# Kernel tuning notes

Measured on AMD Instinct MI355X. Metric: run time of the kernel, lower is better.

Reference implementation:

```python
import jax, jax.numpy as jnp
import numpy as np

B, C, H, W, K = 2, 64, 192, 192, 7
PAD = K // 2
EPS = 1e-6


def _win_idx(L):
    # NATTEN border handling: window is shifted (not zero-padded) to stay in-bounds.
    i = jnp.arange(L)
    start = jnp.clip(i - PAD, 0, L - K)            # [L] window start per query pos
    win = start[:, None] + jnp.arange(K)[None]     # [L,K] absolute key positions
    pb = (K - 1) - (i - start)                     # [L] rpb start index per query pos
    pbi = pb[:, None] + jnp.arange(K)[None]        # [L,K] rpb table indices
    return win, pbi


def setup_inputs() -> dict:
    key = jax.random.key(0)
    ks = jax.random.split(key, 10)
    g = jax.random.normal(ks[0], (B, C, H, W), jnp.float32)
    cd = jax.random.uniform(ks[1], (B, 1, H, W), dtype=jnp.float32)
    dense = jax.random.uniform(ks[2], (B, 1, H, W), dtype=jnp.float32)
    sel = jax.random.uniform(ks[3], (B, 1, H, W)) < 0.05
    sd = jnp.where(sel, dense, 0.0)
    mask = (jax.random.uniform(ks[4], (B, 1, H, W)) < 0.5).astype(jnp.float32)
    ln_w = 1.0 + 0.02 * jax.random.normal(ks[5], (C,), jnp.float32)
    ln_b = 0.02 * jax.random.normal(ks[6], (C,), jnp.float32)
    conv_w = 0.05 * jax.random.normal(ks[7], (2 * C, C + 1), jnp.float32)  # 1x1 conv
    conv_b = 0.02 * jax.random.normal(ks[8], (2 * C,), jnp.float32)
    rpb = 0.02 * jax.random.normal(ks[9], (1, 2 * K - 1, 2 * K - 1), jnp.float32)
    return {"g": g, "cd": cd, "sd": sd, "mask": mask,
            "ln_w": ln_w, "ln_b": ln_b, "conv_w": conv_w, "conv_b": conv_b, "rpb": rpb}


def reference(g, cd, sd, mask, ln_w, ln_b, conv_w, conv_b, rpb):
    # LayerNorm2d: normalize over channel dim per spatial location
    mu = g.mean(axis=1, keepdims=True)
    var = ((g - mu) ** 2).mean(axis=1, keepdims=True)
    gn = (g - mu) * jax.lax.rsqrt(var + EPS)
    gn = gn * ln_w[None, :, None, None] + ln_b[None, :, None, None]

    z = jnp.concatenate([gn, cd], axis=1)                      # [B,C+1,H,W]
    qk = jnp.einsum('bchw,oc->bohw', z, conv_w) + conv_b[None, :, None, None]
    q, k = qk[:, :C], qk[:, C:]
    k = k * mask

    qc = q.transpose(0, 2, 3, 1)                               # [B,H,W,C] single head
    kc = k.transpose(0, 2, 3, 1)
    rwin, rpbi = _win_idx(H)
    cwin, cpbi = _win_idx(W)

    # NATTEN qk + relative position bias over 7x7 neighborhoods
    k_win = kc[:, rwin][:, :, :, cwin]                         # [B,H,K,W,K,C]
    attn = jnp.einsum('bhwc,bhiwjc->bhwij', qc, k_win)         # [B,H,W,K,K]
    bias = rpb[0][rpbi][:, :, cpbi]                            # [H,K,W,K]
    attn = attn + bias.transpose(0, 2, 1, 3)[None]
    a = jax.nn.softmax(attn.reshape(B, H, W, K * K), axis=-1).reshape(B, H, W, K, K)

    # NATTEN av with v = cd (head_dim 1)
    v_win = cd[:, 0][:, rwin][:, :, :, cwin]                   # [B,H,K,W,K]
    cd_out = jnp.einsum('bhwij,bhiwj->bhw', a, v_win)[:, None]  # [B,1,H,W]
    m_win = mask[:, 0][:, rwin][:, :, :, cwin]
    mask_out = jnp.einsum('bhwij,bhiwj->bhw', a, m_win)[:, None]

    # NYU / SDR post-processing
    cd_out = cd_out * mask + cd * (1.0 - mask)
    valid = sd > 0
    cd_out = jnp.where(valid, sd, cd_out)
    mask_out = jnp.where(valid, mask, mask_out)
    return cd_out, mask_out
```

## Files before the change

kernel.cpp:

```cpp
#include <hip/hip_runtime.h>

constexpr int NB = 2;
constexpr int NC = 64;
constexpr int NH = 192;
constexpr int NW = 192;
constexpr int NK = 7;
constexpr int NHW = NH * NW;
constexpr int NPIX = NB * NHW;
constexpr float EPS = 1e-6f;

__global__ __launch_bounds__(256) void qk_gemm(
    const float* __restrict__ g, const float* __restrict__ cd,
    const float* __restrict__ mask,
    const float* __restrict__ ln_w, const float* __restrict__ ln_b,
    const float* __restrict__ conv_w, const float* __restrict__ conv_b,
    float* __restrict__ qbuf, float* __restrict__ kbuf)
{
    __shared__ float Z[65][128];
    __shared__ float WTc[33][128];

    int tid = threadIdx.x;
    int p0 = blockIdx.x * 128;
    int b  = p0 / NHW;
    int hw0 = p0 - b * NHW;

    int px = tid >> 1;
    int hf = tid & 1;
    const float* gp = g + (size_t)(b * NC + hf * 32) * NHW + (hw0 + px);
    float vals[32];
    float s = 0.f, sq = 0.f;
#pragma unroll
    for (int j = 0; j < 32; ++j) {
        float v = gp[(size_t)j * NHW];
        vals[j] = v; s += v; sq += v * v;
    }
    s  += __shfl_xor(s, 1);
    sq += __shfl_xor(sq, 1);
    float mu   = s * (1.f / 64.f);
    float rstd = rsqrtf(sq * (1.f / 64.f) - mu * mu + EPS);
#pragma unroll
    for (int j = 0; j < 32; ++j) {
        int c = hf * 32 + j;
        Z[c][px] = (vals[j] - mu) * rstd * ln_w[c] + ln_b[c];
    }
    if (hf) Z[64][px] = cd[p0 + px];

    int og = tid >> 4;
    int pg = tid & 15;
    float acc[8][8];
#pragma unroll
    for (int oi = 0; oi < 8; ++oi)
#pragma unroll
        for (int pj = 0; pj < 8; ++pj) acc[oi][pj] = 0.f;

    for (int cc = 0; cc < 65; cc += 33) {
        int nr = (65 - cc < 33) ? (65 - cc) : 33;
        __syncthreads();
        if (tid < 128) {
            int o = tid;
            for (int r = 0; r < nr; ++r)
                WTc[r][o] = conv_w[o * 65 + cc + r];
        }
        __syncthreads();
        for (int r = 0; r < nr; ++r) {
            float4 w0 = *(const float4*)&WTc[r][8 * og];
            float4 w1 = *(const float4*)&WTc[r][8 * og + 4];
            float4 z0 = *(const float4*)&Z[cc + r][8 * pg];
            float4 z1 = *(const float4*)&Z[cc + r][8 * pg + 4];
            float w8[8] = {w0.x, w0.y, w0.z, w0.w, w1.x, w1.y, w1.z, w1.w};
            float z8[8] = {z0.x, z0.y, z0.z, z0.w, z1.x, z1.y, z1.z, z1.w};
#pragma unroll
            for (int oi = 0; oi < 8; ++oi)
#pragma unroll
                for (int pj = 0; pj < 8; ++pj)
                    acc[oi][pj] = fmaf(w8[oi], z8[pj], acc[oi][pj]);
        }
    }

    int o0  = og * 8;
    int pxb = pg * 8;
    float4 ba = *(const float4*)&conv_b[o0];
    float4 bb = *(const float4*)&conv_b[o0 + 4];
    float bia[8] = {ba.x, ba.y, ba.z, ba.w, bb.x, bb.y, bb.z, bb.w};
    bool isq = (o0 < 64);
    float m8[8];
    if (!isq) {
        float4 ma = *(const float4*)&mask[p0 + pxb];
        float4 mc = *(const float4*)&mask[p0 + pxb + 4];
        m8[0]=ma.x; m8[1]=ma.y; m8[2]=ma.z; m8[3]=ma.w;
        m8[4]=mc.x; m8[5]=mc.y; m8[6]=mc.z; m8[7]=mc.w;
    }
    float* base = isq ? (qbuf + (size_t)(b * NC + o0) * NHW + hw0 + pxb)
                      : (kbuf + (size_t)(b * NC + o0 - 64) * NHW + hw0 + pxb);
#pragma unroll
    for (int oi = 0; oi < 8; ++oi) {
        float v[8];
#pragma unroll
        for (int pj = 0; pj < 8; ++pj) {
            float t = acc[oi][pj] + bia[oi];
            v[pj] = isq ? t : t * m8[pj];
        }
        float* dst = base + (size_t)oi * NHW;
        *(float4*)&dst[0] = make_float4(v[0], v[1], v[2], v[3]);
        *(float4*)&dst[4] = make_float4(v[4], v[5], v[6], v[7]);
    }
}

__global__ __launch_bounds__(256) void attn_tile(
    const float* __restrict__ qbuf, const float* __restrict__ kbuf,
    const float* __restrict__ cd, const float* __restrict__ sd,
    const float* __restrict__ mask, const float* __restrict__ rpb,
    float* __restrict__ out_cd, float* __restrict__ out_mask)
{
    __shared__ float kst[4][2][10 * 24];
    __shared__ float cdt[14 * 24];
    __shared__ float mt [14 * 24];
    __shared__ float rpbt[169];
    __shared__ float xch[128][49];

    int tid  = threadIdx.x;
    int g    = tid >> 6;
    int lane = tid & 63;
    int rq   = g & 1;
    int half = g >> 1;
    int tx   = lane & 15;
    int tyw  = lane >> 4;

    int bw = blockIdx.x % 12;
    int t2 = blockIdx.x / 12;
    int bh = t2 % 24;
    int b  = t2 / 24;
    int w0 = bw * 16, h0 = bh * 8;
    int hr0 = h0 + rq * 4;

    int h = hr0 + tyw;
    int w = w0 + tx;
    int rs = min(max(h - 3, 0), NH - NK);
    int cs = min(max(w - 3, 0), NW - NK);
    int rb  = (rs - (hr0 - 3)) * 24 + (cs - (w0 - 3));
    int rbB = (rs - (h0  - 3)) * 24 + (cs - (w0 - 3));

    const float* cdb = cd   + (size_t)b * NHW;
    const float* msb = mask + (size_t)b * NHW;
    for (int e = tid; e < 308; e += 256) {
        int r = e / 22, c2 = e - r * 22;
        int gr = min(max(h0 - 3 + r, 0), NH - 1);
        int gc = min(max(w0 - 3 + c2, 0), NW - 1);
        cdt[r * 24 + c2] = cdb[gr * NW + gc];
        mt [r * 24 + c2] = msb[gr * NW + gc];
    }
    if (tid < 169) rpbt[tid] = rpb[tid];

    int soff[4], slds[4]; bool sact[4];
#pragma unroll
    for (int s = 0; s < 4; ++s) {
        int e = lane + 64 * s;
        int r = e / 22, c2 = e - r * 22;
        int gr = min(max(hr0 - 3 + r, 0), NH - 1);
        int gc = min(max(w0 - 3 + c2, 0), NW - 1);
        soff[s] = gr * NW + gc;
        slds[s] = r * 24 + c2;
        sact[s] = (e < 220);
    }

    const float* kb = kbuf + (size_t)(b * NC + half * 32) * NHW;
    const float* qb = qbuf + (size_t)(b * NC + half * 32) * NHW + h * NW + w;

    float at[49];
#pragma unroll
    for (int n = 0; n < 49; ++n) at[n] = 0.f;

    float st[4];
#pragma unroll
    for (int s = 0; s < 4; ++s) st[s] = sact[s] ? kb[soff[s]] : 0.f;
    float* k0 = kst[g][0];
    float* k1 = kst[g][1];
#pragma unroll
    for (int s = 0; s < 4; ++s) if (sact[s]) k0[slds[s]] = st[s];

    for (int i = 0; i < 32; ++i) {
        if (i + 1 < 32) {
            const float* kb2 = kb + (size_t)(i + 1) * NHW;
#pragma unroll
            for (int s = 0; s < 4; ++s) st[s] = sact[s] ? kb2[soff[s]] : 0.f;
        }
        float q = qb[(size_t)i * NHW];
        const float* kt = ((i & 1) ? k1 : k0) + rb;
#pragma unroll
        for (int r = 0; r < 7; ++r)
#pragma unroll
            for (int j = 0; j < 7; ++j)
                at[r * 7 + j] = fmaf(q, kt[r * 24 + j], at[r * 7 + j]);
        if (i + 1 < 32) {
            float* nk = (i & 1) ? k0 : k1;
#pragma unroll
            for (int s = 0; s < 4; ++s) if (sact[s]) nk[slds[s]] = st[s];
        }
    }

    int pxid = (rq * 4 + tyw) * 16 + tx;
    __syncthreads();
    if (half == 1) {
#pragma unroll
        for (int n = 0; n < 49; ++n) xch[pxid][n] = at[n];
    }
    __syncthreads();
    int pr = 6 - (h - rs);
    int pc = 6 - (w - cs);
    if (half == 0) {
#pragma unroll
        for (int n = 0; n < 49; ++n) at[n] += xch[pxid][n];
#pragma unroll
        for (int r = 0; r < 7; ++r)
#pragma unroll
            for (int j = 0; j < 7; ++j)
                at[r * 7 + j] += rpbt[(pr + r) * 13 + pc + j];
#pragma unroll
        for (int n = 0; n < 49; ++n) xch[pxid][n] = at[n];
    }
    __syncthreads();
    if (half == 1) {
#pragma unroll
        for (int n = 0; n < 49; ++n) at[n] = xch[pxid][n];
    }

    float mx = -1e30f;
#pragma unroll
    for (int n = 0; n < 49; ++n) mx = fmaxf(mx, at[n]);
    float sm = 0.f;
#pragma unroll
    for (int n = 0; n < 49; ++n) {
        at[n] = __expf(at[n] - mx);
        sm += at[n];
    }

    const float* vt = (half ? mt : cdt) + rbB;
    float sv = 0.f;
#pragma unroll
    for (int r = 0; r < 7; ++r)
#pragma unroll
        for (int j = 0; j < 7; ++j)
            sv = fmaf(at[r * 7 + j], vt[r * 24 + j], sv);
    sv /= sm;

    int p = b * NHW + h * NW + w;
    float sdc = sd[p];
    int cidx = (rq * 4 + tyw + 3) * 24 + (tx + 3);
    float mc = mt[cidx];
    if (half == 0) {
        float cdc = cdt[cidx];
        float co = sv * mc + cdc * (1.f - mc);
        if (sdc > 0.f) co = sdc;
        out_cd[p] = co;
    } else {
        out_mask[p] = (sdc > 0.f) ? mc : sv;
    }
}

extern "C" void kernel_launch(void* const* d_in, const int* in_sizes, int n_in,
                              void* d_out, int out_size, void* d_ws, size_t ws_size,
                              hipStream_t stream) {
    const float* g      = (const float*)d_in[0];
    const float* cd     = (const float*)d_in[1];
    const float* sd     = (const float*)d_in[2];
    const float* mask   = (const float*)d_in[3];
    const float* ln_w   = (const float*)d_in[4];
    const float* ln_b   = (const float*)d_in[5];
    const float* conv_w = (const float*)d_in[6];
    const float* conv_b = (const float*)d_in[7];
    const float* rpb    = (const float*)d_in[8];

    float* out  = (float*)d_out;
    float* qbuf = (float*)d_ws;
    float* kbuf = qbuf + (size_t)NB * NC * NHW;

    qk_gemm<<<dim3(NPIX / 128), dim3(256), 0, stream>>>(
        g, cd, mask, ln_w, ln_b, conv_w, conv_b, qbuf, kbuf);
    attn_tile<<<dim3(NB * 24 * 12), dim3(256), 0, stream>>>(
        qbuf, kbuf, cd, sd, mask, rpb, out, out + NPIX);
}
```

Measured before the change: 140.7 us.

## Replace shared-memory attention tile with per-wave DPP lane-shift neighborhood kernel

The neighborhood attention kernel is rewritten so that each wave handles one image row segment of 48 output pixels, using 64 lanes with an 8-lane halo on each side. Horizontal neighbors come from DPP row-shift moves instead of shared-memory tiles. Each thread now loops over all 64 channels itself, removing the split across two halves, the exchange buffer and the block barriers. Border columns use templated modes that compute extra shifted products and select the right window. This trades LDS traffic and sync for redundant halo lanes (25% wasted), more direct global loads of K rows, and higher register pressure.

```diff
diff --git a/kernel.cpp b/kernel.cpp
--- a/kernel.cpp
+++ b/kernel.cpp
@@ -106,155 +106,224 @@
     }
 }
 
-__global__ __launch_bounds__(256) void attn_tile(
+__device__ inline float dpp_p1(float x) {
+    return __int_as_float(__builtin_amdgcn_mov_dpp(
+        __float_as_int(x), 0x130, 0xf, 0xf, true));
+}
+__device__ inline float dpp_m1(float x) {
+    return __int_as_float(__builtin_amdgcn_mov_dpp(
+        __float_as_int(x), 0x138, 0xf, 0xf, true));
+}
+
+template <int MODE>
+__device__ void attn_wave(
+    int b, int h, int s, int lane,
     const float* __restrict__ qbuf, const float* __restrict__ kbuf,
     const float* __restrict__ cd, const float* __restrict__ sd,
     const float* __restrict__ mask, const float* __restrict__ rpb,
     float* __restrict__ out_cd, float* __restrict__ out_mask)
 {
-    __shared__ float kst[4][2][10 * 24];
-    __shared__ float cdt[14 * 24];
-    __shared__ float mt [14 * 24];
-    __shared__ float rpbt[169];
-    __shared__ float xch[128][49];
-
-    int tid  = threadIdx.x;
-    int g    = tid >> 6;
-    int lane = tid & 63;
-    int rq   = g & 1;
-    int half = g >> 1;
-    int tx   = lane & 15;
-    int tyw  = lane >> 4;
-
-    int bw = blockIdx.x % 12;
-    int t2 = blockIdx.x / 12;
-    int bh = t2 % 24;
-    int b  = t2 / 24;
-    int w0 = bw * 16, h0 = bh * 8;
-    int hr0 = h0 + rq * 4;
-
-    int h = hr0 + tyw;
-    int w = w0 + tx;
+    int w0 = s * 48;
+    int wp = w0 + lane - 8;
+    int wc = min(max(wp, 0), NW - 1);
     int rs = min(max(h - 3, 0), NH - NK);
-    int cs = min(max(w - 3, 0), NW - NK);
-    int rb  = (rs - (hr0 - 3)) * 24 + (cs - (w0 - 3));
-    int rbB = (rs - (h0  - 3)) * 24 + (cs - (w0 - 3));
+    int pr = 6 - (h - rs);
+
+    const float* kb = kbuf + (size_t)b * NC * NHW;
+    const float* qb = qbuf + (size_t)b * NC * NHW + h * NW + wc;
+
+    float at[49];
+#pragma unroll
+    for (int n = 0; n < 49; ++n) at[n] = 0.f;
+    float ax[21];
+    if (MODE != 0) {
+#pragma unroll
+        for (int n = 0; n < 21; ++n) ax[n] = 0.f;
+    }
+
+    float q0 = qb[0];
+    float q1 = qb[(size_t)1 * NHW];
+    float q2 = qb[(size_t)2 * NHW];
+    float q3 = qb[(size_t)3 * NHW];
+    float kvA[7], kvB[7];
+#pragma unroll
+    for (int r = 0; r < 7; ++r) kvA[r] = kb[(rs + r) * NW + wc];
+
+    auto loadrow = [&](float (&dst)[7], int c) {
+        const float* p = kb + (size_t)c * NHW;
+#pragma unroll
+        for (int r = 0; r < 7; ++r) dst[r] = p[(rs + r) * NW + wc];
+    };
+    auto compute = [&](float (&cur)[7], float qc) {
+#pragma unroll
+        for (int r = 0; r < 7; ++r) {
+            float t0 = cur[r];
+            float p1 = dpp_p1(t0), p2 = dpp_p1(p1), p3 = dpp_p1(p2);
+            float m1 = dpp_m1(t0), m2 = dpp_m1(m1), m3 = dpp_m1(m2);
+            at[r*7+0] = fmaf(qc, m3, at[r*7+0]);
+            at[r*7+1] = fmaf(qc, m2, at[r*7+1]);
+            at[r*7+2] = fmaf(qc, m1, at[r*7+2]);
+            at[r*7+3] = fmaf(qc, t0, at[r*7+3]);
+            at[r*7+4] = fmaf(qc, p1, at[r*7+4]);
+            at[r*7+5] = fmaf(qc, p2, at[r*7+5]);
+            at[r*7+6] = fmaf(qc, p3, at[r*7+6]);
+            if (MODE == 1) {
+                float p4 = dpp_p1(p3), p5 = dpp_p1(p4), p6 = dpp_p1(p5);
+                ax[r*3+0] = fmaf(qc, p4, ax[r*3+0]);
+                ax[r*3+1] = fmaf(qc, p5, ax[r*3+1]);
+                ax[r*3+2] = fmaf(qc, p6, ax[r*3+2]);
+            }
+            if (MODE == 2) {
+                float m4 = dpp_m1(m3), m5 = dpp_m1(m4), m6 = dpp_m1(m5);
+                ax[r*3+0] = fmaf(qc, m4, ax[r*3+0]);
+                ax[r*3+1] = fmaf(qc, m5, ax[r*3+1]);
+                ax[r*3+2] = fmaf(qc, m6, ax[r*3+2]);
+            }
+        }
+    };
+
+    for (int c = 0; c < 64; c += 4) {
+        if (c + 1 < 64) loadrow(kvB, c + 1);
+        compute(kvA, q0);
+        if (c + 4 < 64) q0 = qb[(size_t)(c + 4) * NHW];
+        if (c + 2 < 64) loadrow(kvA, c + 2);
+        compute(kvB, q1);
+        if (c + 5 < 64) q1 = qb[(size_t)(c + 5) * NHW];
+        if (c + 3 < 64) loadrow(kvB, c + 3);
+        compute(kvA, q2);
+        if (c + 6 < 64) q2 = qb[(size_t)(c + 6) * NHW];
+        if (c + 4 < 64) loadrow(kvA, c + 4);
+        compute(kvB, q3);
+        if (c + 7 < 64) q3 = qb[(size_t)(c + 7) * NHW];
+    }
+
+    int cs = min(max(wp - 3, 0), NW - NK);
+    int e  = cs - (wp - 3);
+    if (MODE == 1) {
+#pragma unroll
+        for (int i = 0; i < 7; ++i)
+#pragma unroll
+            for (int j = 0; j < 7; ++j) {
+                float v = at[i*7+j];
+                v = (e >= 1) ? ((j+1 <= 6) ? at[i*7+j+1] : ax[i*3+j-6]) : v;
+                v = (e >= 2) ? ((j+2 <= 6) ? at[i*7+j+2] : ax[i*3+j-5]) : v;
+                v = (e >= 3) ? ((j+3 <= 6) ? at[i*7+j+3] : ax[i*3+j-4]) : v;
+                at[i*7+j] = v;
+            }
+    }
+    if (MODE == 2) {
+#pragma unroll
+        for (int i = 0; i < 7; ++i)
+#pragma unroll
+            for (int jj = 6; jj >= 0; --jj) {
+                int j = jj;
+                float v = at[i*7+j];
+                v = (e <= -1) ? ((j >= 1) ? at[i*7+j-1] : ax[i*3+0]) : v;
+                v = (e <= -2) ? ((j >= 2) ? at[i*7+j-2] : ax[i*3+1-j]) : v;
+                v = (e <= -3) ? ((j >= 3) ? at[i*7+j-3] : ax[i*3+2-j]) : v;
+                at[i*7+j] = v;
+            }
+    }
+
+    int pc = 3 + e;
+    const float* rp = rpb + pr * 13 + pc;
+#pragma unroll
+    for (int i = 0; i < 7; ++i)
+#pragma unroll
+        for (int j = 0; j < 7; ++j)
+            at[i*7+j] += rp[i * 13 + j];
+
+    float mx = -1e30f;
+#pragma unroll
+    for (int n = 0; n < 49; ++n) mx = fmaxf(mx, at[n]);
+    float sm = 0.f;
+#pragma unroll
+    for (int n = 0; n < 49; ++n) { at[n] = __expf(at[n] - mx); sm += at[n]; }
+    float inv = 1.f / sm;
 
     const float* cdb = cd   + (size_t)b * NHW;
     const float* msb = mask + (size_t)b * NHW;
-    for (int e = tid; e < 308; e += 256) {
-        int r = e / 22, c2 = e - r * 22;
-        int gr = min(max(h0 - 3 + r, 0), NH - 1);
-        int gc = min(max(w0 - 3 + c2, 0), NW - 1);
-        cdt[r * 24 + c2] = cdb[gr * NW + gc];
-        mt [r * 24 + c2] = msb[gr * NW + gc];
-    }
-    if (tid < 169) rpbt[tid] = rpb[tid];
-
-    int soff[4], slds[4]; bool sact[4];
-#pragma unroll
-    for (int s = 0; s < 4; ++s) {
-        int e = lane + 64 * s;
-        int r = e / 22, c2 = e - r * 22;
-        int gr = min(max(hr0 - 3 + r, 0), NH - 1);
-        int gc = min(max(w0 - 3 + c2, 0), NW - 1);
-        soff[s] = gr * NW + gc;
-        slds[s] = r * 24 + c2;
-        sact[s] = (e < 220);
-    }
-
-    const float* kb = kbuf + (size_t)(b * NC + half * 32) * NHW;
-    const float* qb = qbuf + (size_t)(b * NC + half * 32) * NHW + h * NW + w;
-
-    float at[49];
-#pragma unroll
-    for (int n = 0; n < 49; ++n) at[n] = 0.f;
-
-    float st[4];
-#pragma unroll
-    for (int s = 0; s < 4; ++s) st[s] = sact[s] ? kb[soff[s]] : 0.f;
-    float* k0 = kst[g][0];
-    float* k1 = kst[g][1];
-#pragma unroll
-    for (int s = 0; s < 4; ++s) if (sact[s]) k0[slds[s]] = st[s];
-
-    for (int i = 0; i < 32; ++i) {
-        if (i + 1 < 32) {
-            const float* kb2 = kb + (size_t)(i + 1) * NHW;
-#pragma unroll
-            for (int s = 0; s < 4; ++s) st[s] = sact[s] ? kb2[soff[s]] : 0.f;
-        }
-        float q = qb[(size_t)i * NHW];
-        const float* kt = ((i & 1) ? k1 : k0) + rb;
-#pragma unroll
-        for (int r = 0; r < 7; ++r)
-#pragma unroll
-            for (int j = 0; j < 7; ++j)
-                at[r * 7 + j] = fmaf(q, kt[r * 24 + j], at[r * 7 + j]);
-        if (i + 1 < 32) {
-            float* nk = (i & 1) ? k0 : k1;
-#pragma unroll
-            for (int s = 0; s < 4; ++s) if (sact[s]) nk[slds[s]] = st[s];
-        }
-    }
-
-    int pxid = (rq * 4 + tyw) * 16 + tx;
-    __syncthreads();
-    if (half == 1) {
-#pragma unroll
-        for (int n = 0; n < 49; ++n) xch[pxid][n] = at[n];
-    }
-    __syncthreads();
-    int pr = 6 - (h - rs);
-    int pc = 6 - (w - cs);
-    if (half == 0) {
-#pragma unroll
-        for (int n = 0; n < 49; ++n) at[n] += xch[pxid][n];
-#pragma unroll
-        for (int r = 0; r < 7; ++r)
-#pragma unroll
-            for (int j = 0; j < 7; ++j)
-                at[r * 7 + j] += rpbt[(pr + r) * 13 + pc + j];
-#pragma unroll
-        for (int n = 0; n < 49; ++n) xch[pxid][n] = at[n];
-    }
-    __syncthreads();
-    if (half == 1) {
-#pragma unroll
-        for (int n = 0; n < 49; ++n) at[n] = xch[pxid][n];
-    }
-
-    float mx = -1e30f;
-#pragma unroll
-    for (int n = 0; n < 49; ++n) mx = fmaxf(mx, at[n]);
-    float sm = 0.f;
-#pragma unroll
-    for (int n = 0; n < 49; ++n) {
-        at[n] = __expf(at[n] - mx);
-        sm += at[n];
-    }
-
-    const float* vt = (half ? mt : cdt) + rbB;
-    float sv = 0.f;
-#pragma unroll
-    for (int r = 0; r < 7; ++r)
-#pragma unroll
-        for (int j = 0; j < 7; ++j)
-            sv = fmaf(at[r * 7 + j], vt[r * 24 + j], sv);
-    sv /= sm;
-
-    int p = b * NHW + h * NW + w;
-    float sdc = sd[p];
-    int cidx = (rq * 4 + tyw + 3) * 24 + (tx + 3);
-    float mc = mt[cidx];
-    if (half == 0) {
-        float cdc = cdt[cidx];
-        float co = sv * mc + cdc * (1.f - mc);
-        if (sdc > 0.f) co = sdc;
+    float oc = 0.f, om = 0.f;
+#pragma unroll
+    for (int r = 0; r < 7; ++r) {
+        float c0 = cdb[(rs + r) * NW + wc];
+        float m0 = msb[(rs + r) * NW + wc];
+        float cp1 = dpp_p1(c0), cp2 = dpp_p1(cp1), cp3 = dpp_p1(cp2);
+        float cm1 = dpp_m1(c0), cm2 = dpp_m1(cm1), cm3 = dpp_m1(cm2);
+        float mp1 = dpp_p1(m0), mp2 = dpp_p1(mp1), mp3 = dpp_p1(mp2);
+        float mm1 = dpp_m1(m0), mm2 = dpp_m1(mm1), mm3 = dpp_m1(mm2);
+        float cw[7] = {cm3, cm2, cm1, c0, cp1, cp2, cp3};
+        float mw[7] = {mm3, mm2, mm1, m0, mp1, mp2, mp3};
+        if (MODE == 1) {
+            float cp4 = dpp_p1(cp3), cp5 = dpp_p1(cp4), cp6 = dpp_p1(cp5);
+            float mp4 = dpp_p1(mp3), mp5 = dpp_p1(mp4), mp6 = dpp_p1(mp5);
+            float cx[10] = {cm3,cm2,cm1,c0,cp1,cp2,cp3,cp4,cp5,cp6};
+            float mxw[10] = {mm3,mm2,mm1,m0,mp1,mp2,mp3,mp4,mp5,mp6};
+#pragma unroll
+            for (int j = 0; j < 7; ++j) {
+                float v = cx[j], u = mxw[j];
+                v = (e >= 1) ? cx[j+1] : v;  u = (e >= 1) ? mxw[j+1] : u;
+                v = (e >= 2) ? cx[j+2] : v;  u = (e >= 2) ? mxw[j+2] : u;
+                v = (e >= 3) ? cx[j+3] : v;  u = (e >= 3) ? mxw[j+3] : u;
+                cw[j] = v; mw[j] = u;
+            }
+        }
+        if (MODE == 2) {
+            float cm4 = dpp_m1(cm3), cm5 = dpp_m1(cm4), cm6 = dpp_m1(cm5);
+            float mm4 = dpp_m1(mm3), mm5 = dpp_m1(mm4), mm6 = dpp_m1(mm5);
+            float cx[10] = {cm6,cm5,cm4,cm3,cm2,cm1,c0,cp1,cp2,cp3};
+            float mxw[10] = {mm6,mm5,mm4,mm3,mm2,mm1,m0,mp1,mp2,mp3};
+#pragma unroll
+            for (int j = 0; j < 7; ++j) {
+                float v = cx[j+3], u = mxw[j+3];
+                v = (e <= -1) ? cx[j+2] : v;  u = (e <= -1) ? mxw[j+2] : u;
+                v = (e <= -2) ? cx[j+1] : v;  u = (e <= -2) ? mxw[j+1] : u;
+                v = (e <= -3) ? cx[j+0] : v;  u = (e <= -3) ? mxw[j+0] : u;
+                cw[j] = v; mw[j] = u;
+            }
+        }
+#pragma unroll
+        for (int j = 0; j < 7; ++j) {
+            oc = fmaf(at[r*7+j], cw[j], oc);
+            om = fmaf(at[r*7+j], mw[j], om);
+        }
+    }
+    oc *= inv; om *= inv;
+
+    float cdc = cdb[h * NW + wc];
+    float mc  = msb[h * NW + wc];
+    float sdc = sd[(size_t)b * NHW + h * NW + wc];
+    float co = oc * mc + cdc * (1.f - mc);
+    float mo = om;
+    if (sdc > 0.f) { co = sdc; mo = mc; }
+    if (lane >= 8 && lane < 56) {
+        int p = b * NHW + h * NW + wp;
         out_cd[p] = co;
-    } else {
-        out_mask[p] = (sdc > 0.f) ? mc : sv;
-    }
+        out_mask[p] = mo;
+    }
+}
+
+__global__ __launch_bounds__(256) void attn_dpp(
+    const float* __restrict__ qbuf, const float* __restrict__ kbuf,
+    const float* __restrict__ cd, const float* __restrict__ sd,
+    const float* __restrict__ mask, const float* __restrict__ rpb,
+    float* __restrict__ out_cd, float* __restrict__ out_mask)
+{
+    int tid  = threadIdx.x;
+    int lane = tid & 63;
+    int wave = tid >> 6;
+    int blk = blockIdx.x;
+    int b   = blk / 192;
+    int r2  = blk % 192;
+    int s   = r2 / 48;
+    int h   = (r2 % 48) * 4 + wave;
+
+    if (s == 0)
+        attn_wave<1>(b, h, s, lane, qbuf, kbuf, cd, sd, mask, rpb, out_cd, out_mask);
+    else if (s == 3)
+        attn_wave<2>(b, h, s, lane, qbuf, kbuf, cd, sd, mask, rpb, out_cd, out_mask);
+    else
+        attn_wave<0>(b, h, s, lane, qbuf, kbuf, cd, sd, mask, rpb, out_cd, out_mask);
 }
 
 extern "C" void kernel_launch(void* const* d_in, const int* in_sizes, int n_in,
@@ -276,6 +345,6 @@
 
     qk_gemm<<<dim3(NPIX / 128), dim3(256), 0, stream>>>(
         g, cd, mask, ln_w, ln_b, conv_w, conv_b, qbuf, kbuf);
-    attn_tile<<<dim3(NB * 24 * 12), dim3(256), 0, stream>>>(
+    attn_dpp<<<dim3(NB * 192), dim3(256), 0, stream>>>(
         qbuf, kbuf, cd, sd, mask, rpb, out, out + NPIX);
 }
```

Result: slower. 171.5 us (+21.9%).
